# Kernel tuning notes

Hardware: AMD Instinct MI355X
Metric: run time of the kernel (lower is better)

Reference implementation:

```python
import jax, jax.numpy as jnp
import numpy as np

B, N, D, H = 1, 512, 128, 128  # batch, seq, pair dim, hidden dim
EPS = 1e-6  # flax nnx LayerNorm default epsilon


def _layernorm(x, scale, bias):
    m = jnp.mean(x, axis=-1, keepdims=True)
    v = jnp.var(x, axis=-1, keepdims=True)
    return (x - m) * jax.lax.rsqrt(v + EPS) * scale + bias


def setup_inputs() -> dict:
    key = jax.random.key(0)
    ks = jax.random.split(key, 12)
    s = 0.02  # param init scale
    inp = {
        "x": jax.random.normal(ks[0], (B, N, N, D), jnp.float32),
        "src_mask": jnp.ones((B, N), jnp.float32),
        # first LayerNorm
        "ln1_scale": jnp.ones((D,), jnp.float32),
        "ln1_bias": jnp.zeros((D,), jnp.float32),
        # left/right projections
        "wl": jax.random.normal(ks[1], (D, H), jnp.float32) * s,
        "bl": jnp.zeros((H,), jnp.float32),
        "wr": jax.random.normal(ks[2], (D, H), jnp.float32) * s,
        "br": jnp.zeros((H,), jnp.float32),
        # gates (original inits kernel=0, bias=1; use small random kernels + bias=1 for a nontrivial baseline)
        "wlg": jax.random.normal(ks[3], (D, H), jnp.float32) * s,
        "blg": jnp.ones((H,), jnp.float32),
        "wrg": jax.random.normal(ks[4], (D, H), jnp.float32) * s,
        "brg": jnp.ones((H,), jnp.float32),
        "wog": jax.random.normal(ks[5], (D, H), jnp.float32) * s,
        "bog": jnp.ones((H,), jnp.float32),
        # output LayerNorm + projection
        "ln2_scale": jnp.ones((H,), jnp.float32),
        "ln2_bias": jnp.zeros((H,), jnp.float32),
        "wo": jax.random.normal(ks[6], (H, D), jnp.float32) * s,
        "bo": jnp.zeros((D,), jnp.float32),
    }
    return inp


def reference(x, src_mask, ln1_scale, ln1_bias, wl, bl, wr, br, wlg, blg,
              wrg, brg, wog, bog, ln2_scale, ln2_bias, wo, bo):
    # mask[b,i,j] = src_mask[b,i] * src_mask[b,j]  -> [B,N,N,1]
    sm = src_mask.astype(jnp.float32)
    mask = (sm[:, :, None] * sm[:, None, :])[..., None]

    xn = _layernorm(x, ln1_scale, ln1_bias)  # [B,N,N,D]

    # projections, mask, gates (gating after transpose in the original is
    # elementwise, hence equivalent applied pre-transpose)
    left = (xn @ wl + bl) * mask * jax.nn.sigmoid(xn @ wlg + blg)   # [B,N,N,H]
    right = (xn @ wr + br) * mask * jax.nn.sigmoid(xn @ wrg + brg)  # [B,N,N,H]
    out_gate = jax.nn.sigmoid(xn @ wog + bog)                       # [B,N,N,H]

    # 'ingoing' mix: out[b,i,j,d] = sum_k left[b,k,i,d] * right[b,k,j,d]
    out = jnp.einsum('bkid,bkjd->bijd', left, right)

    out = _layernorm(out, ln2_scale, ln2_bias) * out_gate
    return out @ wo + bo
```

## Files before the change

kernel.cpp:

```cpp
#include <hip/hip_runtime.h>
#include <hip/hip_bf16.h>


#define NSEQ 512
#define NN 262144
#define DMODEL 128

typedef __attribute__((ext_vector_type(8))) short short8;
typedef __attribute__((ext_vector_type(4))) float f32x4;

__device__ __forceinline__ unsigned short f2b(float f) {
    __hip_bfloat16 h = __float2bfloat16(f);
    return *reinterpret_cast<unsigned short*>(&h);
}
__device__ __forceinline__ float b2f(unsigned short u) {
    __hip_bfloat16 h;
    *reinterpret_cast<unsigned short*>(&h) = u;
    return __bfloat162float(h);
}
__device__ __forceinline__ float sigmoidf_(float x) {
    return 1.0f / (1.0f + __expf(-x));
}

__global__ __launch_bounds__(256) void k_wt_all(
    const float* __restrict__ w0, const float* __restrict__ w1,
    const float* __restrict__ w2, const float* __restrict__ w3,
    const float* __restrict__ w4, const float* __restrict__ w5,
    unsigned short* __restrict__ wt) {
    int bid = blockIdx.x;
    int mat = bid >> 6;
    const float* w = (mat == 0) ? w0 : (mat == 1) ? w1 : (mat == 2) ? w2
                   : (mat == 3) ? w3 : (mat == 4) ? w4 : w5;
    int idx = (bid & 63) * 256 + threadIdx.x;
    int d = idx >> 7, h = idx & 127;
    wt[mat * 16384 + h * 128 + d] = f2b(w[idx]);
}

__global__ __launch_bounds__(256) void k_proj(
    const float* __restrict__ x,
    const float* __restrict__ src_mask,
    const float* __restrict__ ln1s, const float* __restrict__ ln1b,
    const unsigned short* __restrict__ wt,
    const float* __restrict__ bl,  const float* __restrict__ blg,
    const float* __restrict__ br,  const float* __restrict__ brg,
    const float* __restrict__ bog,
    unsigned short* __restrict__ left_t,
    unsigned short* __restrict__ right_t,
    unsigned short* __restrict__ og) {
    __shared__ __align__(16) unsigned short As[64 * 136];
    const int t = threadIdx.x;
    const int lane = t & 63;
    const int wv = t >> 6;
    const int a0 = blockIdx.x * 64;
    const int b  = blockIdx.y;
    const int n0 = wv * 32;

    {
        int row = t >> 2, seg = t & 3;
        const float* px = x + ((size_t)(a0 + row) * NSEQ + b) * DMODEL + seg * 32;
        float4 xv[8];
        float s = 0.f, sq = 0.f;
        #pragma unroll
        for (int i = 0; i < 8; ++i) {
            xv[i] = *(const float4*)(px + i * 4);
            s  += xv[i].x + xv[i].y + xv[i].z + xv[i].w;
            sq += xv[i].x * xv[i].x + xv[i].y * xv[i].y
                + xv[i].z * xv[i].z + xv[i].w * xv[i].w;
        }
        s  += __shfl_xor(s, 1);  s  += __shfl_xor(s, 2);
        sq += __shfl_xor(sq, 1); sq += __shfl_xor(sq, 2);
        float mean = s * (1.f / 128.f);
        float var  = sq * (1.f / 128.f) - mean * mean;
        float inv  = rsqrtf(var + 1e-6f);
        #pragma unroll
        for (int v = 0; v < 4; ++v) {
            short8 o;
            #pragma unroll
            for (int e = 0; e < 8; ++e) {
                int d = seg * 32 + v * 8 + e;
                float xe = ((const float*)&xv[v * 2 + (e >> 2)])[e & 3];
                o[e] = (short)f2b((xe - mean) * inv * ln1s[d] + ln1b[d]);
            }
            *(short8*)(&As[row * 136 + seg * 32 + v * 8]) = o;
        }
    }
    __syncthreads();

    short8 af[4][4];
    #pragma unroll
    for (int mf = 0; mf < 4; ++mf)
        #pragma unroll
        for (int kc = 0; kc < 4; ++kc)
            af[mf][kc] = *(const short8*)(
                &As[(mf * 16 + (lane & 15)) * 136 + kc * 32 + (lane >> 4) * 8]);

    short8 bfA[2][4], bfB[2][4];
    f32x4 acc0[4][2], acc1[4][2];
    float smb = src_mask[b];

    auto loadB = [&](short8 (&dst)[2][4], int mat) {
        #pragma unroll
        for (int nf = 0; nf < 2; ++nf)
            #pragma unroll
            for (int kc = 0; kc < 4; ++kc)
                dst[nf][kc] = *(const short8*)(
                    wt + mat * 16384 + (n0 + nf * 16 + (lane & 15)) * 128
                       + kc * 32 + (lane >> 4) * 8);
    };
    auto mmat = [&](f32x4 (&acc)[4][2], short8 (&bf)[2][4]) {
        #pragma unroll
        for (int mf = 0; mf < 4; ++mf)
            #pragma unroll
            for (int nf = 0; nf < 2; ++nf)
                acc[mf][nf] = f32x4{0.f, 0.f, 0.f, 0.f};
        #pragma unroll
        for (int kc = 0; kc < 4; ++kc)
            #pragma unroll
            for (int mf = 0; mf < 4; ++mf)
                #pragma unroll
                for (int nf = 0; nf < 2; ++nf)
                    acc[mf][nf] = __builtin_amdgcn_mfma_f32_16x16x32_bf16(
                        af[mf][kc], bf[nf][kc], acc[mf][nf], 0, 0, 0);
    };
    auto epi_pair = [&](const float* b1, const float* b2, unsigned short* dst) {
        #pragma unroll
        for (int nf = 0; nf < 2; ++nf) {
            int h = n0 + nf * 16 + (lane & 15);
            float b1v = b1[h], b2v = b2[h];
            #pragma unroll
            for (int mf = 0; mf < 4; ++mf) {
                int abase = a0 + mf * 16 + ((lane >> 4) << 2);
                unsigned long long pv64 = 0;
                #pragma unroll
                for (int j = 0; j < 4; ++j) {
                    float pv = acc0[mf][nf][j] + b1v;
                    float gv = acc1[mf][nf][j] + b2v;
                    float mk = src_mask[abase + j] * smb;
                    unsigned long long q = f2b(pv * mk * sigmoidf_(gv));
                    pv64 |= q << (16 * j);
                }
                *(unsigned long long*)(dst + (size_t)h * NN + (size_t)b * NSEQ + abase) = pv64;
            }
        }
    };

    loadB(bfA, 0);
    loadB(bfB, 1);
    mmat(acc0, bfA);
    loadB(bfA, 2);
    mmat(acc1, bfB);
    loadB(bfB, 3);
    epi_pair(bl, blg, left_t);
    mmat(acc0, bfA);
    loadB(bfA, 4);
    mmat(acc1, bfB);
    epi_pair(br, brg, right_t);
    mmat(acc0, bfA);
    #pragma unroll
    for (int nf = 0; nf < 2; ++nf) {
        int h = n0 + nf * 16 + (lane & 15);
        float bv = bog[h];
        #pragma unroll
        for (int mf = 0; mf < 4; ++mf) {
            int abase = a0 + mf * 16 + ((lane >> 4) << 2);
            #pragma unroll
            for (int j = 0; j < 4; ++j) {
                float ov = sigmoidf_(acc0[mf][nf][j] + bv);
                og[((size_t)(abase + j) * NSEQ + b) * DMODEL + h] = f2b(ov);
            }
        }
    }
}

__global__ __launch_bounds__(256) void k_einsum(
    const unsigned short* __restrict__ lt,
    const unsigned short* __restrict__ rt,
    unsigned short* __restrict__ mid) {
    __shared__ __align__(16) unsigned short As[128 * 40];
    __shared__ __align__(16) unsigned short Bs[128 * 40];
    const int t = threadIdx.x, lane = t & 63, wv = t >> 6;
    const int d = blockIdx.z;
    const int i0 = blockIdx.x * 128, j0 = blockIdx.y * 128;
    const int m0 = (wv >> 1) * 64, n0 = (wv & 1) * 64;
    const unsigned short* Ag = lt + (size_t)d * NN;
    const unsigned short* Bg = rt + (size_t)d * NN;

    f32x4 acc[4][4];
    #pragma unroll
    for (int mf = 0; mf < 4; ++mf)
        #pragma unroll
        for (int nf = 0; nf < 4; ++nf)
            acc[mf][nf] = f32x4{0.f, 0.f, 0.f, 0.f};

    for (int k0 = 0; k0 < NSEQ; k0 += 32) {
        __syncthreads();
        for (int it = 0; it < 2; ++it) {
            int idx = it * 256 + t;
            int row = idx >> 2, c = idx & 3;
            *(short8*)(&As[row * 40 + c * 8]) =
                *(const short8*)(Ag + (size_t)(i0 + row) * NSEQ + k0 + c * 8);
            *(short8*)(&Bs[row * 40 + c * 8]) =
                *(const short8*)(Bg + (size_t)(j0 + row) * NSEQ + k0 + c * 8);
        }
        __syncthreads();
        int ko = (lane >> 4) * 8;
        short8 af[4], bf[4];
        #pragma unroll
        for (int mf = 0; mf < 4; ++mf)
            af[mf] = *(const short8*)(&As[(m0 + mf * 16 + (lane & 15)) * 40 + ko]);
        #pragma unroll
        for (int nf = 0; nf < 4; ++nf)
            bf[nf] = *(const short8*)(&Bs[(n0 + nf * 16 + (lane & 15)) * 40 + ko]);
        #pragma unroll
        for (int mf = 0; mf < 4; ++mf)
            #pragma unroll
            for (int nf = 0; nf < 4; ++nf)
                acc[mf][nf] = __builtin_amdgcn_mfma_f32_16x16x32_bf16(
                    af[mf], bf[nf], acc[mf][nf], 0, 0, 0);
    }
    unsigned short* out = mid + (size_t)d * NN;
    #pragma unroll
    for (int mf = 0; mf < 4; ++mf) {
        int rbase = i0 + m0 + mf * 16 + ((lane >> 4) << 2);
        #pragma unroll
        for (int nf = 0; nf < 4; ++nf) {
            int col = j0 + n0 + nf * 16 + (lane & 15);
            #pragma unroll
            for (int j = 0; j < 4; ++j)
                out[(size_t)(rbase + j) * NSEQ + col] = f2b(acc[mf][nf][j]);
        }
    }
}

__global__ __launch_bounds__(128) void k_ln2gate(
    const unsigned short* __restrict__ mid,
    const unsigned short* __restrict__ og,
    const float* __restrict__ sc, const float* __restrict__ bi,
    unsigned short* __restrict__ g) {
    __shared__ __align__(16) unsigned short lo[128 * 136];
    const int t = threadIdx.x;
    const size_t p0 = (size_t)blockIdx.x * 128;
    const size_t p = p0 + t;

    unsigned int vals[64];
    float s = 0.f, sq = 0.f;
    #pragma unroll
    for (int d2 = 0; d2 < 64; ++d2) {
        unsigned int a = mid[(size_t)(2 * d2)     * NN + p];
        unsigned int c = mid[(size_t)(2 * d2 + 1) * NN + p];
        vals[d2] = a | (c << 16);
        float fa = b2f((unsigned short)a), fc = b2f((unsigned short)c);
        s += fa + fc; sq += fa * fa + fc * fc;
    }
    float mean = s * (1.f / 128.f);
    float var  = sq * (1.f / 128.f) - mean * mean;
    float inv  = rsqrtf(var + 1e-6f);
    #pragma unroll
    for (int c = 0; c < 16; ++c) {
        short8 ov = *(const short8*)(og + p * DMODEL + c * 8);
        short8 r8;
        #pragma unroll
        for (int e = 0; e < 8; ++e) {
            int d = c * 8 + e;
            unsigned int w = vals[d >> 1];
            float v = b2f((unsigned short)((d & 1) ? (w >> 16) : (w & 0xffff)));
            float y = (v - mean) * inv * sc[d] + bi[d];
            r8[e] = (short)f2b(y * b2f((unsigned short)ov[e]));
        }
        *(short8*)(&lo[t * 136 + c * 8]) = r8;
    }
    __syncthreads();
    #pragma unroll
    for (int i = 0; i < 16; ++i) {
        int idx = i * 128 + t;
        int row = idx >> 4, ch = idx & 15;
        *(short8*)(g + (p0 + row) * DMODEL + ch * 8) =
            *(const short8*)(&lo[row * 136 + ch * 8]);
    }
}

__global__ __launch_bounds__(256) void k_out(
    const unsigned short* __restrict__ g,
    const unsigned short* __restrict__ wt_o,
    const float* __restrict__ bo,
    float* __restrict__ out) {
    __shared__ __align__(16) unsigned short As[64 * 136];
    __shared__ __align__(16) unsigned short Bs[128 * 136];
    const int t = threadIdx.x, lane = t & 63, wv = t >> 6;
    const size_t r0 = (size_t)blockIdx.x * 64;
    const int n0 = wv * 32;
    for (int it = 0; it < 4; ++it) {
        int idx = it * 256 + t;
        int row = idx >> 4, c = idx & 15;
        *(short8*)(&As[row * 136 + c * 8]) =
            *(const short8*)(g + (r0 + row) * DMODEL + c * 8);
    }
    for (int it = 0; it < 8; ++it) {
        int idx = it * 256 + t;
        int h = idx >> 4, c = idx & 15;
        *(short8*)(&Bs[h * 136 + c * 8]) = *(const short8*)(wt_o + h * 128 + c * 8);
    }
    __syncthreads();
    f32x4 acc[4][2];
    #pragma unroll
    for (int mf = 0; mf < 4; ++mf)
        #pragma unroll
        for (int nf = 0; nf < 2; ++nf)
            acc[mf][nf] = f32x4{0.f, 0.f, 0.f, 0.f};
    #pragma unroll
    for (int kc = 0; kc < 4; ++kc) {
        int ko = kc * 32 + (lane >> 4) * 8;
        short8 af[4], bf[2];
        #pragma unroll
        for (int mf = 0; mf < 4; ++mf)
            af[mf] = *(const short8*)(&As[(mf * 16 + (lane & 15)) * 136 + ko]);
        #pragma unroll
        for (int nf = 0; nf < 2; ++nf)
            bf[nf] = *(const short8*)(&Bs[(n0 + nf * 16 + (lane & 15)) * 136 + ko]);
        #pragma unroll
        for (int mf = 0; mf < 4; ++mf)
            #pragma unroll
            for (int nf = 0; nf < 2; ++nf)
                acc[mf][nf] = __builtin_amdgcn_mfma_f32_16x16x32_bf16(
                    af[mf], bf[nf], acc[mf][nf], 0, 0, 0);
    }
    #pragma unroll
    for (int nf = 0; nf < 2; ++nf) {
        int n = n0 + nf * 16 + (lane & 15);
        float bv = bo[n];
        #pragma unroll
        for (int mf = 0; mf < 4; ++mf) {
            int rb = mf * 16 + ((lane >> 4) << 2);
            #pragma unroll
            for (int j = 0; j < 4; ++j)
                out[(r0 + rb + j) * DMODEL + n] = acc[mf][nf][j] + bv;
        }
    }
}

extern "C" void kernel_launch(void* const* d_in, const int* in_sizes, int n_in,
                              void* d_out, int out_size, void* d_ws, size_t ws_size,
                              hipStream_t stream) {
    const float* x    = (const float*)d_in[0];
    const float* sm   = (const float*)d_in[1];
    const float* ln1s = (const float*)d_in[2];
    const float* ln1b = (const float*)d_in[3];
    const float* wl   = (const float*)d_in[4];
    const float* bl   = (const float*)d_in[5];
    const float* wr   = (const float*)d_in[6];
    const float* br   = (const float*)d_in[7];
    const float* wlg  = (const float*)d_in[8];
    const float* blg  = (const float*)d_in[9];
    const float* wrg  = (const float*)d_in[10];
    const float* brg  = (const float*)d_in[11];
    const float* wog  = (const float*)d_in[12];
    const float* bog  = (const float*)d_in[13];
    const float* ln2s = (const float*)d_in[14];
    const float* ln2b = (const float*)d_in[15];
    const float* wo   = (const float*)d_in[16];
    const float* bo   = (const float*)d_in[17];
    float* out = (float*)d_out;

    char* ws = (char*)d_ws;
    unsigned short* wt  = (unsigned short*)ws;
    unsigned short* lt  = (unsigned short*)(ws + 196608);
    unsigned short* rt  = (unsigned short*)(ws + 196608 + 1ull * 67108864);
    unsigned short* ogb = (unsigned short*)(ws + 196608 + 2ull * 67108864);
    unsigned short* mid = (unsigned short*)(ws + 196608 + 3ull * 67108864);
    unsigned short* gb  = (unsigned short*)(ws + 196608 + 4ull * 67108864);

    k_wt_all<<<384, 256, 0, stream>>>(wl, wlg, wr, wrg, wog, wo, wt);
    k_proj<<<dim3(8, 512), 256, 0, stream>>>(x, sm, ln1s, ln1b, wt,
                                             bl, blg, br, brg, bog, lt, rt, ogb);
    k_einsum<<<dim3(4, 4, 128), 256, 0, stream>>>(lt, rt, mid);
    k_ln2gate<<<2048, 128, 0, stream>>>(mid, ogb, ln2s, ln2b, gb);
    k_out<<<4096, 256, 0, stream>>>(gb, wt + 5 * 16384, bo, out);
}
```

Measured before the change: 358.8 us.

## Split LayerNorm into separate kernel, remap einsum blocks per XCD, shrink LDS padding

Adds a standalone k_ln1 kernel that writes a bf16 normalized copy of x. k_proj then loads its A fragments directly from global memory instead of staging them through shared memory, and gets a launch-bounds hint of two blocks per CU. The einsum grid becomes 1D with blockIdx remapped so that each XCD handles a contiguous range of d slices, aiming at better L2 locality, and LDS row padding drops from 40 to 36. The extra pass costs one more read of the fp32 input plus a 64MB bf16 write and reread. Row stride 36 may also introduce LDS bank conflicts.

```diff
diff --git a/kernel.cpp b/kernel.cpp
--- a/kernel.cpp
+++ b/kernel.cpp
@@ -36,10 +36,37 @@
     wt[mat * 16384 + h * 128 + d] = f2b(w[idx]);
 }
 
-__global__ __launch_bounds__(256) void k_proj(
-    const float* __restrict__ x,
+__global__ __launch_bounds__(256) void k_ln1(const float* __restrict__ x,
+                                             const float* __restrict__ sc,
+                                             const float* __restrict__ bi,
+                                             unsigned short* __restrict__ xn) {
+    int t = threadIdx.x;
+    int l = t & 31;
+    size_t row = (size_t)blockIdx.x * 8 + (t >> 5);
+    float4 v = *(const float4*)(x + row * DMODEL + l * 4);
+    float s  = v.x + v.y + v.z + v.w;
+    float sq = v.x * v.x + v.y * v.y + v.z * v.z + v.w * v.w;
+    #pragma unroll
+    for (int m = 1; m < 32; m <<= 1) {
+        s  += __shfl_xor(s, m);
+        sq += __shfl_xor(sq, m);
+    }
+    float mean = s * (1.f / 128.f);
+    float var  = sq * (1.f / 128.f) - mean * mean;
+    float inv  = rsqrtf(var + 1e-6f);
+    float4 scv = *(const float4*)(sc + l * 4);
+    float4 biv = *(const float4*)(bi + l * 4);
+    unsigned long long o = 0;
+    o |= (unsigned long long)f2b((v.x - mean) * inv * scv.x + biv.x);
+    o |= (unsigned long long)f2b((v.y - mean) * inv * scv.y + biv.y) << 16;
+    o |= (unsigned long long)f2b((v.z - mean) * inv * scv.z + biv.z) << 32;
+    o |= (unsigned long long)f2b((v.w - mean) * inv * scv.w + biv.w) << 48;
+    *(unsigned long long*)(xn + row * DMODEL + l * 4) = o;
+}
+
+__global__ __launch_bounds__(256, 2) void k_proj(
+    const unsigned short* __restrict__ xn,
     const float* __restrict__ src_mask,
-    const float* __restrict__ ln1s, const float* __restrict__ ln1b,
     const unsigned short* __restrict__ wt,
     const float* __restrict__ bl,  const float* __restrict__ blg,
     const float* __restrict__ br,  const float* __restrict__ brg,
@@ -47,7 +74,6 @@
     unsigned short* __restrict__ left_t,
     unsigned short* __restrict__ right_t,
     unsigned short* __restrict__ og) {
-    __shared__ __align__(16) unsigned short As[64 * 136];
     const int t = threadIdx.x;
     const int lane = t & 63;
     const int wv = t >> 6;
@@ -55,58 +81,33 @@
     const int b  = blockIdx.y;
     const int n0 = wv * 32;
 
+    short8 bfA[2][4], bfB[2][4];
+    auto loadB = [&](short8 (&dst)[2][4], int mat) {
+        const unsigned short* base = wt + mat * 16384 + (lane >> 4) * 8;
+        #pragma unroll
+        for (int nf = 0; nf < 2; ++nf)
+            #pragma unroll
+            for (int kc = 0; kc < 4; ++kc)
+                dst[nf][kc] = *(const short8*)(
+                    base + (n0 + nf * 16 + (lane & 15)) * 128 + kc * 32);
+    };
+    loadB(bfA, 0);
+    loadB(bfB, 1);
+
+    short8 af[4][4];
     {
-        int row = t >> 2, seg = t & 3;
-        const float* px = x + ((size_t)(a0 + row) * NSEQ + b) * DMODEL + seg * 32;
-        float4 xv[8];
-        float s = 0.f, sq = 0.f;
-        #pragma unroll
-        for (int i = 0; i < 8; ++i) {
-            xv[i] = *(const float4*)(px + i * 4);
-            s  += xv[i].x + xv[i].y + xv[i].z + xv[i].w;
-            sq += xv[i].x * xv[i].x + xv[i].y * xv[i].y
-                + xv[i].z * xv[i].z + xv[i].w * xv[i].w;
-        }
-        s  += __shfl_xor(s, 1);  s  += __shfl_xor(s, 2);
-        sq += __shfl_xor(sq, 1); sq += __shfl_xor(sq, 2);
-        float mean = s * (1.f / 128.f);
-        float var  = sq * (1.f / 128.f) - mean * mean;
-        float inv  = rsqrtf(var + 1e-6f);
-        #pragma unroll
-        for (int v = 0; v < 4; ++v) {
-            short8 o;
-            #pragma unroll
-            for (int e = 0; e < 8; ++e) {
-                int d = seg * 32 + v * 8 + e;
-                float xe = ((const float*)&xv[v * 2 + (e >> 2)])[e & 3];
-                o[e] = (short)f2b((xe - mean) * inv * ln1s[d] + ln1b[d]);
-            }
-            *(short8*)(&As[row * 136 + seg * 32 + v * 8]) = o;
-        }
-    }
-    __syncthreads();
-
-    short8 af[4][4];
-    #pragma unroll
-    for (int mf = 0; mf < 4; ++mf)
-        #pragma unroll
-        for (int kc = 0; kc < 4; ++kc)
-            af[mf][kc] = *(const short8*)(
-                &As[(mf * 16 + (lane & 15)) * 136 + kc * 32 + (lane >> 4) * 8]);
-
-    short8 bfA[2][4], bfB[2][4];
+        const unsigned short* abase =
+            xn + ((size_t)(a0 + (lane & 15)) * NSEQ + b) * DMODEL + (lane >> 4) * 8;
+        #pragma unroll
+        for (int mf = 0; mf < 4; ++mf)
+            #pragma unroll
+            for (int kc = 0; kc < 4; ++kc)
+                af[mf][kc] = *(const short8*)(abase + (size_t)mf * 16 * NSEQ * DMODEL + kc * 32);
+    }
+
     f32x4 acc0[4][2], acc1[4][2];
     float smb = src_mask[b];
 
-    auto loadB = [&](short8 (&dst)[2][4], int mat) {
-        #pragma unroll
-        for (int nf = 0; nf < 2; ++nf)
-            #pragma unroll
-            for (int kc = 0; kc < 4; ++kc)
-                dst[nf][kc] = *(const short8*)(
-                    wt + mat * 16384 + (n0 + nf * 16 + (lane & 15)) * 128
-                       + kc * 32 + (lane >> 4) * 8);
-    };
     auto mmat = [&](f32x4 (&acc)[4][2], short8 (&bf)[2][4]) {
         #pragma unroll
         for (int mf = 0; mf < 4; ++mf)
@@ -144,8 +145,6 @@
         }
     };
 
-    loadB(bfA, 0);
-    loadB(bfB, 1);
     mmat(acc0, bfA);
     loadB(bfA, 2);
     mmat(acc1, bfB);
@@ -176,11 +175,14 @@
     const unsigned short* __restrict__ lt,
     const unsigned short* __restrict__ rt,
     unsigned short* __restrict__ mid) {
-    __shared__ __align__(16) unsigned short As[128 * 40];
-    __shared__ __align__(16) unsigned short Bs[128 * 40];
+    __shared__ __align__(16) unsigned short As[128 * 36];
+    __shared__ __align__(16) unsigned short Bs[128 * 36];
     const int t = threadIdx.x, lane = t & 63, wv = t >> 6;
-    const int d = blockIdx.z;
-    const int i0 = blockIdx.x * 128, j0 = blockIdx.y * 128;
+    const int bid = blockIdx.x;
+    const int xcd = bid & 7, slot = bid >> 3;
+    const int d = xcd * 16 + (slot >> 4);
+    const int tile = slot & 15;
+    const int i0 = (tile >> 2) * 128, j0 = (tile & 3) * 128;
     const int m0 = (wv >> 1) * 64, n0 = (wv & 1) * 64;
     const unsigned short* Ag = lt + (size_t)d * NN;
     const unsigned short* Bg = rt + (size_t)d * NN;
@@ -194,23 +196,24 @@
 
     for (int k0 = 0; k0 < NSEQ; k0 += 32) {
         __syncthreads();
+        #pragma unroll
         for (int it = 0; it < 2; ++it) {
-            int idx = it * 256 + t;
-            int row = idx >> 2, c = idx & 3;
-            *(short8*)(&As[row * 40 + c * 8]) =
-                *(const short8*)(Ag + (size_t)(i0 + row) * NSEQ + k0 + c * 8);
-            *(short8*)(&Bs[row * 40 + c * 8]) =
-                *(const short8*)(Bg + (size_t)(j0 + row) * NSEQ + k0 + c * 8);
+            int c = it * 256 + t;
+            int row = c >> 2, sub = c & 3;
+            *(short8*)(&As[row * 36 + sub * 8]) =
+                *(const short8*)(Ag + (size_t)(i0 + row) * NSEQ + k0 + sub * 8);
+            *(short8*)(&Bs[row * 36 + sub * 8]) =
+                *(const short8*)(Bg + (size_t)(j0 + row) * NSEQ + k0 + sub * 8);
         }
         __syncthreads();
         int ko = (lane >> 4) * 8;
         short8 af[4], bf[4];
         #pragma unroll
         for (int mf = 0; mf < 4; ++mf)
-            af[mf] = *(const short8*)(&As[(m0 + mf * 16 + (lane & 15)) * 40 + ko]);
+            af[mf] = *(const short8*)(&As[(m0 + mf * 16 + (lane & 15)) * 36 + ko]);
         #pragma unroll
         for (int nf = 0; nf < 4; ++nf)
-            bf[nf] = *(const short8*)(&Bs[(n0 + nf * 16 + (lane & 15)) * 40 + ko]);
+            bf[nf] = *(const short8*)(&Bs[(n0 + nf * 16 + (lane & 15)) * 36 + ko]);
         #pragma unroll
         for (int mf = 0; mf < 4; ++mf)
             #pragma unroll
@@ -363,16 +366,18 @@
 
     char* ws = (char*)d_ws;
     unsigned short* wt  = (unsigned short*)ws;
-    unsigned short* lt  = (unsigned short*)(ws + 196608);
-    unsigned short* rt  = (unsigned short*)(ws + 196608 + 1ull * 67108864);
-    unsigned short* ogb = (unsigned short*)(ws + 196608 + 2ull * 67108864);
-    unsigned short* mid = (unsigned short*)(ws + 196608 + 3ull * 67108864);
-    unsigned short* gb  = (unsigned short*)(ws + 196608 + 4ull * 67108864);
+    unsigned short* xn  = (unsigned short*)(ws + 196608);
+    unsigned short* lt  = (unsigned short*)(ws + 196608 + 1ull * 67108864);
+    unsigned short* rt  = (unsigned short*)(ws + 196608 + 2ull * 67108864);
+    unsigned short* ogb = (unsigned short*)(ws + 196608 + 3ull * 67108864);
+    unsigned short* mid = (unsigned short*)(ws + 196608 + 4ull * 67108864);
+    unsigned short* gb  = xn;
 
     k_wt_all<<<384, 256, 0, stream>>>(wl, wlg, wr, wrg, wog, wo, wt);
-    k_proj<<<dim3(8, 512), 256, 0, stream>>>(x, sm, ln1s, ln1b, wt,
+    k_ln1<<<32768, 256, 0, stream>>>(x, ln1s, ln1b, xn);
+    k_proj<<<dim3(8, 512), 256, 0, stream>>>(xn, sm, wt,
                                              bl, blg, br, brg, bog, lt, rt, ogb);
-    k_einsum<<<dim3(4, 4, 128), 256, 0, stream>>>(lt, rt, mid);
+    k_einsum<<<2048, 256, 0, stream>>>(lt, rt, mid);
     k_ln2gate<<<2048, 128, 0, stream>>>(mid, ogb, ln2s, ln2b, gb);
     k_out<<<4096, 256, 0, stream>>>(gb, wt + 5 * 16384, bo, out);
 }
```

Result: slower. 392.4 us (+9.4%).
